# Kernel optimization log

Measured on AMD Instinct MI355X. Metric: run time of the kernel, lower is better.

The kernel has to match this reference:

```python
import jax, jax.numpy as jnp
import numpy as np

D_MODEL = 1024
NUM_HEADS = 16
D_K = D_MODEL // NUM_HEADS


def setup_inputs() -> dict:
    key = jax.random.key(0)
    k1, k2, k3 = jax.random.split(key, 3)
    x = jax.random.normal(k1, (2, 2048, D_MODEL), dtype=jnp.float32)
    # torch Linear(d, 3d): weight shape [3d, d], y = x @ W.T
    W_QKV = jax.random.normal(k2, (3 * D_MODEL, D_MODEL), dtype=jnp.float32) * (1.0 / np.sqrt(D_MODEL))
    W_O = jax.random.normal(k3, (D_MODEL, D_MODEL), dtype=jnp.float32) * (1.0 / np.sqrt(D_MODEL))
    return {"x": x, "W_QKV": W_QKV, "W_O": W_O}


def reference(x, W_QKV, W_O):
    B, T, C = x.shape
    qkv = jnp.einsum('btc,fc->btf', x, W_QKV)  # [B,T,3C]
    q, k, v = jnp.split(qkv, 3, axis=-1)
    def heads(t):
        return t.reshape(B, T, NUM_HEADS, D_K).transpose(0, 2, 1, 3)  # [B,H,T,Dk]
    Q, K, V = heads(q), heads(k), heads(v)
    scores = jnp.einsum('bhqd,bhkd->bhqk', Q, K) / jnp.sqrt(jnp.float32(D_K))
    causal = jnp.tril(jnp.ones((T, T), dtype=bool))
    scores = jnp.where(causal, scores, -jnp.inf)
    attn = jax.nn.softmax(scores, axis=-1)
    out = jnp.einsum('bhqk,bhkd->bhqd', attn, V)
    out = out.transpose(0, 2, 1, 3).reshape(B, T, C)
    return jnp.einsum('btc,oc->bto', out, W_O)
```

## Files before the change

kernel.cpp:

```cpp
#include <hip/hip_runtime.h>
#include <hip/hip_bf16.h>
#include <stdint.h>
#include <stddef.h>


typedef __attribute__((ext_vector_type(8)))  __bf16   bf16x8;
typedef __attribute__((ext_vector_type(4)))  float    f32x4;
typedef __attribute__((ext_vector_type(16))) float    f32x16;
typedef __attribute__((ext_vector_type(4)))  uint32_t u32x4;

#define AS1(p) ((__attribute__((address_space(1))) void*)(p))
#define AS3(p) ((__attribute__((address_space(3))) void*)(p))

static constexpr int Tq    = 2048;
static constexpr int Cd    = 1024;
static constexpr int Mrows = 2 * Tq;

#define QSCALE 0.18033688011112042f

__global__ __launch_bounds__(256) void cvt_bf16_kernel(const float* __restrict__ in,
                                                       __bf16* __restrict__ out, int n8)
{
    int idx    = blockIdx.x * blockDim.x + threadIdx.x;
    int stride = gridDim.x * blockDim.x;
    for (int i = idx; i < n8; i += stride) {
        f32x4 a = ((const f32x4*)in)[i * 2 + 0];
        f32x4 b = ((const f32x4*)in)[i * 2 + 1];
        bf16x8 o;
#pragma unroll
        for (int j = 0; j < 4; ++j) { o[j] = (__bf16)a[j]; o[4 + j] = (__bf16)b[j]; }
        ((bf16x8*)out)[i] = o;
    }
}

__global__ __launch_bounds__(256) void transpose_v_kernel(const __bf16* __restrict__ qkv,
                                                          __bf16* __restrict__ vT)
{
    __shared__ __bf16 tile[64][65];
    const int t   = threadIdx.x;
    const int r0  = blockIdx.x * 64;
    const int hd0 = blockIdx.y * 64;

    {
        const int rr = t >> 2, c16 = (t & 3) * 16;
        const __bf16* src = qkv + (size_t)(r0 + rr) * 3072 + 2048 + hd0 + c16;
        bf16x8 a = *(const bf16x8*)(src);
        bf16x8 b = *(const bf16x8*)(src + 8);
#pragma unroll
        for (int j = 0; j < 8; ++j) { tile[rr][c16 + j] = a[j]; tile[rr][c16 + 8 + j] = b[j]; }
    }
    __syncthreads();
    {
        const int hd_loc = t >> 2, rg = (t & 3) * 16;
        bf16x8 a, b;
#pragma unroll
        for (int j = 0; j < 8; ++j) { a[j] = tile[rg + j][hd_loc]; b[j] = tile[rg + 8 + j][hd_loc]; }
        __bf16* dst = vT + (size_t)(hd0 + hd_loc) * Mrows + r0 + rg;
        *(bf16x8*)(dst)     = a;
        *(bf16x8*)(dst + 8) = b;
    }
}

template <bool OUT_BF16>
__global__ __launch_bounds__(256) void gemm_bt_kernel(const __bf16* __restrict__ A,
                                                      const __bf16* __restrict__ Bm,
                                                      float* __restrict__ Cf,
                                                      __bf16* __restrict__ Cb,
                                                      int N, int K, int qcols, float qscale)
{
    __shared__ __align__(16) __bf16 As[128 * 64];
    __shared__ __align__(16) __bf16 Bs[128 * 64];

    const int tid = threadIdx.x;
    const int l   = tid & 63;
    const int w   = tid >> 6;
    const int wr  = w >> 1, wc = w & 1;
    const int lo  = l & 15, hi = l >> 4;
    const int m0  = blockIdx.x * 128;
    const int n0  = blockIdx.y * 128;

    f32x4 acc[4][4] = {};

    for (int kk = 0; kk < K; kk += 64) {
#pragma unroll
        for (int i = 0; i < 4; ++i) {
            int s   = i * 256 + tid;
            int row = s >> 3;
            int gg  = (s & 7) ^ (row & 7);
            const __bf16* srcA = A  + (size_t)(m0 + row) * K + kk + gg * 8;
            const __bf16* srcB = Bm + (size_t)(n0 + row) * K + kk + gg * 8;
            __builtin_amdgcn_global_load_lds(AS1(srcA), AS3((char*)As + s * 16), 16, 0, 0);
            __builtin_amdgcn_global_load_lds(AS1(srcB), AS3((char*)Bs + s * 16), 16, 0, 0);
        }
        __syncthreads();

#pragma unroll
        for (int ks = 0; ks < 2; ++ks) {
            bf16x8 af[4], bfr[4];
#pragma unroll
            for (int m = 0; m < 4; ++m) {
                int row = wr * 64 + m * 16 + lo;
                int gl  = (ks * 4 + hi) ^ (row & 7);
                af[m] = *(const bf16x8*)((const char*)As + row * 128 + gl * 16);
            }
#pragma unroll
            for (int n = 0; n < 4; ++n) {
                int row = wc * 64 + n * 16 + lo;
                int gl  = (ks * 4 + hi) ^ (row & 7);
                bfr[n] = *(const bf16x8*)((const char*)Bs + row * 128 + gl * 16);
            }
#pragma unroll
            for (int m = 0; m < 4; ++m)
#pragma unroll
                for (int n = 0; n < 4; ++n)
                    acc[m][n] = __builtin_amdgcn_mfma_f32_16x16x32_bf16(af[m], bfr[n], acc[m][n], 0, 0, 0);
        }
        __syncthreads();
    }

#pragma unroll
    for (int m = 0; m < 4; ++m)
#pragma unroll
        for (int n = 0; n < 4; ++n)
#pragma unroll
            for (int r = 0; r < 4; ++r) {
                int row = m0 + wr * 64 + m * 16 + hi * 4 + r;
                int col = n0 + wc * 64 + n * 16 + lo;
                float v = acc[m][n][r];
                if (col < qcols) v *= qscale;
                if (OUT_BF16) Cb[(size_t)row * N + col] = (__bf16)v;
                else          Cf[(size_t)row * N + col] = v;
            }
}

__global__ __launch_bounds__(128) void attn_kernel(const __bf16* __restrict__ qkv,
                                                   const __bf16* __restrict__ vT,
                                                   __bf16* __restrict__ att)
{
    __shared__ __align__(16) __bf16 Ks[2][64 * 64];
    __shared__ __align__(16) __bf16 Vs[2][64 * 64];

    const int tid = threadIdx.x;
    const int l   = tid & 63;
    const int w   = tid >> 6;
    const int lo5 = l & 31, hi5 = l >> 5;

    const int bid = blockIdx.x;
    const int j   = bid & 15;
    const int h   = (bid >> 4) & 15;
    const int b   = bid >> 8;

    const __bf16* Kbase = qkv + (size_t)b * Tq * 3072 + 1024 + h * 64;
    const __bf16* Vbase = vT  + (size_t)h * 64 * Mrows + b * Tq;

    const int qts[2] = {31 - j, j};

    for (int p = 0; p < 2; ++p) {
        const int qt  = qts[p];
        const int qb0 = qt * 64;
        const int nt  = qt + 1;

        bf16x8 qf[4];
        {
            const __bf16* Qp = qkv + (size_t)(b * Tq + qb0 + w * 32 + lo5) * 3072 + h * 64 + hi5 * 8;
#pragma unroll
            for (int ds = 0; ds < 4; ++ds) qf[ds] = *(const bf16x8*)(Qp + ds * 16);
        }

        f32x16 o0 = {}, o1 = {};
        float m = -1e30f, lsum = 0.f;

#pragma unroll
        for (int i = 0; i < 4; ++i) {
            int s = i * 128 + tid;
            int row = s >> 3, g = (s & 7) ^ (row & 7);
            __builtin_amdgcn_global_load_lds(AS1(Kbase + (size_t)row * 3072 + g * 8),
                                             AS3((char*)Ks[0] + s * 16), 16, 0, 0);
            __builtin_amdgcn_global_load_lds(AS1(Vbase + (size_t)row * Mrows + g * 8),
                                             AS3((char*)Vs[0] + s * 16), 16, 0, 0);
        }
        __syncthreads();

        int cur = 0;
        for (int t = 0; t < nt; ++t) {
            const int k0 = t * 64;

            if (t + 1 < nt) {
                const int kn = k0 + 64;
#pragma unroll
                for (int i = 0; i < 4; ++i) {
                    int s = i * 128 + tid;
                    int row = s >> 3, g = (s & 7) ^ (row & 7);
                    __builtin_amdgcn_global_load_lds(AS1(Kbase + (size_t)(kn + row) * 3072 + g * 8),
                                                     AS3((char*)Ks[cur ^ 1] + s * 16), 16, 0, 0);
                    __builtin_amdgcn_global_load_lds(AS1(Vbase + (size_t)row * Mrows + kn + g * 8),
                                                     AS3((char*)Vs[cur ^ 1] + s * 16), 16, 0, 0);
                }
            }

            f32x16 sf0 = {}, sf1 = {};
#pragma unroll
            for (int ds = 0; ds < 4; ++ds) {
                {
                    int row = lo5;
                    int gl  = (ds * 2 + hi5) ^ (row & 7);
                    bf16x8 kf = *(const bf16x8*)((const char*)Ks[cur] + row * 128 + gl * 16);
                    sf0 = __builtin_amdgcn_mfma_f32_32x32x16_bf16(kf, qf[ds], sf0, 0, 0, 0);
                }
                {
                    int row = 32 + lo5;
                    int gl  = (ds * 2 + hi5) ^ (row & 7);
                    bf16x8 kf = *(const bf16x8*)((const char*)Ks[cur] + row * 128 + gl * 16);
                    sf1 = __builtin_amdgcn_mfma_f32_32x32x16_bf16(kf, qf[ds], sf1, 0, 0, 0);
                }
            }

            if (t == qt) {
                const int ql = w * 32 + lo5;
#pragma unroll
                for (int r = 0; r < 16; ++r) {
                    int kc = (r & 3) + 8 * (r >> 2) + 4 * hi5;
                    if (kc      > ql) sf0[r] = -1e30f;
                    if (kc + 32 > ql) sf1[r] = -1e30f;
                }
            }

            float pmh = fmaxf(sf0[0], sf0[1]);
#pragma unroll
            for (int r = 2; r < 16; ++r) pmh = fmaxf(pmh, sf0[r]);
#pragma unroll
            for (int r = 0; r < 16; ++r) pmh = fmaxf(pmh, sf1[r]);
            float pm = fmaxf(pmh, __shfl_xor(pmh, 32));

            if (__any(pm > m + 8.0f)) {
                float mnew = fmaxf(m, pm);
                float fac  = exp2f(m - mnew);
                m = mnew;
                lsum *= fac;
#pragma unroll
                for (int r = 0; r < 16; ++r) {
                    int qreg = (r & 3) + 8 * (r >> 2) + 4 * hi5;
                    float fr = __shfl(fac, qreg);
                    o0[r] *= fr;
                    o1[r] *= fr;
                }
            }

            float psum = 0.f;
#pragma unroll
            for (int kb = 0; kb < 2; ++kb) {
                uint32_t W[8];
#pragma unroll
                for (int wd = 0; wd < 8; ++wd) {
                    float sa = (kb == 0) ? sf0[2 * wd]     : sf1[2 * wd];
                    float sb = (kb == 0) ? sf0[2 * wd + 1] : sf1[2 * wd + 1];
                    float pa = exp2f(sa - m);
                    float pb = exp2f(sb - m);
                    __bf16 ba = (__bf16)pa, bb = (__bf16)pb;
                    psum += (float)ba + (float)bb;
                    W[wd] = (uint32_t)__builtin_bit_cast(uint16_t, ba)
                          | ((uint32_t)__builtin_bit_cast(uint16_t, bb) << 16);
                }
                uint32_t Za = __shfl_xor(hi5 ? W[0] : W[2], 32);
                uint32_t Zb = __shfl_xor(hi5 ? W[1] : W[3], 32);
                uint32_t Zc = __shfl_xor(hi5 ? W[4] : W[6], 32);
                uint32_t Zd = __shfl_xor(hi5 ? W[5] : W[7], 32);

                {
                    u32x4 fw = { hi5 ? Za : W[0], hi5 ? Zb : W[1],
                                 hi5 ? W[2] : Za, hi5 ? W[3] : Zb };
                    bf16x8 pa = __builtin_bit_cast(bf16x8, fw);
                    const int kstep = kb * 2;
                    {
                        int row = lo5;
                        int gl  = (kstep * 2 + hi5) ^ (row & 7);
                        bf16x8 vb = *(const bf16x8*)((const char*)Vs[cur] + row * 128 + gl * 16);
                        o0 = __builtin_amdgcn_mfma_f32_32x32x16_bf16(pa, vb, o0, 0, 0, 0);
                    }
                    {
                        int row = 32 + lo5;
                        int gl  = (kstep * 2 + hi5) ^ (row & 7);
                        bf16x8 vb = *(const bf16x8*)((const char*)Vs[cur] + row * 128 + gl * 16);
                        o1 = __builtin_amdgcn_mfma_f32_32x32x16_bf16(pa, vb, o1, 0, 0, 0);
                    }
                }
                {
                    u32x4 fw = { hi5 ? Zc : W[4], hi5 ? Zd : W[5],
                                 hi5 ? W[6] : Zc, hi5 ? W[7] : Zd };
                    bf16x8 pa = __builtin_bit_cast(bf16x8, fw);
                    const int kstep = kb * 2 + 1;
                    {
                        int row = lo5;
                        int gl  = (kstep * 2 + hi5) ^ (row & 7);
                        bf16x8 vb = *(const bf16x8*)((const char*)Vs[cur] + row * 128 + gl * 16);
                        o0 = __builtin_amdgcn_mfma_f32_32x32x16_bf16(pa, vb, o0, 0, 0, 0);
                    }
                    {
                        int row = 32 + lo5;
                        int gl  = (kstep * 2 + hi5) ^ (row & 7);
                        bf16x8 vb = *(const bf16x8*)((const char*)Vs[cur] + row * 128 + gl * 16);
                        o1 = __builtin_amdgcn_mfma_f32_32x32x16_bf16(pa, vb, o1, 0, 0, 0);
                    }
                }
            }
            psum += __shfl_xor(psum, 32);
            lsum += psum;

            __syncthreads();
            cur ^= 1;
        }

        float linv = 1.0f / lsum;
#pragma unroll
        for (int r = 0; r < 16; ++r) {
            int   qreg = (r & 3) + 8 * (r >> 2) + 4 * hi5;
            float lr   = __shfl(linv, qreg);
            int   rowg = b * Tq + qb0 + w * 32 + qreg;
            att[(size_t)rowg * Cd + h * 64 + lo5]      = (__bf16)(o0[r] * lr);
            att[(size_t)rowg * Cd + h * 64 + 32 + lo5] = (__bf16)(o1[r] * lr);
        }
    }
}

extern "C" void kernel_launch(void* const* d_in, const int* in_sizes, int n_in,
                              void* d_out, int out_size, void* d_ws, size_t ws_size,
                              hipStream_t stream)
{
    (void)in_sizes; (void)n_in; (void)out_size; (void)ws_size;

    const float* x    = (const float*)d_in[0];
    const float* Wqkv = (const float*)d_in[1];
    const float* Wo   = (const float*)d_in[2];
    float*       out  = (float*)d_out;

    char* ws = (char*)d_ws;
    __bf16* xb    = (__bf16*)(ws);
    __bf16* wqkvb = (__bf16*)(ws + (size_t)8  * 1024 * 1024);
    __bf16* wob   = (__bf16*)(ws + (size_t)14 * 1024 * 1024);
    __bf16* qkvb  = (__bf16*)(ws + (size_t)16 * 1024 * 1024);
    __bf16* attb  = (__bf16*)(ws + (size_t)40 * 1024 * 1024);
    __bf16* vTb   = xb;

    cvt_bf16_kernel<<<2048, 256, 0, stream>>>(x,    xb,    Mrows * Cd / 8);
    cvt_bf16_kernel<<<1536, 256, 0, stream>>>(Wqkv, wqkvb, 3 * Cd * Cd / 8);
    cvt_bf16_kernel<<<512,  256, 0, stream>>>(Wo,   wob,   Cd * Cd / 8);

    dim3 g1(Mrows / 128, 3 * Cd / 128);
    gemm_bt_kernel<true><<<g1, 256, 0, stream>>>(xb, wqkvb, nullptr, qkvb, 3 * Cd, Cd,
                                                 1024, QSCALE);

    dim3 gt(Mrows / 64, Cd / 64);
    transpose_v_kernel<<<gt, 256, 0, stream>>>(qkvb, vTb);

    attn_kernel<<<512, 128, 0, stream>>>(qkvb, vTb, attb);

    dim3 g2(Mrows / 128, Cd / 128);
    gemm_bt_kernel<false><<<g2, 256, 0, stream>>>(attb, wob, out, nullptr, Cd, Cd,
                                                  0, 1.0f);
}
```

Baseline: 214.7 us.

## Split attention into one query tile per block, MFMA row sums, setprio

Each attention block now handles a single query tile instead of a paired long/short tile, doubling the grid to 1024 blocks. The query tiles are ordered so the longest causal tiles are scheduled first. The softmax denominator is accumulated with an extra MFMA against a ones vector, replacing scalar adds and shuffles, and the final reciprocal uses rcp. The change also adds s_setprio around the MFMA regions, uses native exp2, and tree-reduces the row max. The trade-off is losing the paired work balancing, relying instead on ordering plus more blocks, and paying extra MFMA work for the row sums.

```diff
diff --git a/kernel.cpp b/kernel.cpp
--- a/kernel.cpp
+++ b/kernel.cpp
@@ -146,179 +146,190 @@
     const int lo5 = l & 31, hi5 = l >> 5;
 
     const int bid = blockIdx.x;
-    const int j   = bid & 15;
-    const int h   = (bid >> 4) & 15;
-    const int b   = bid >> 8;
+    const int g   = (bid >> 5) & 7;
+    const int c   = bid >> 8;
+    const int qt  = (c & 1) ? (16 - ((c >> 1) << 4) + g)
+                            : (31 - ((c >> 1) << 4) - g);
+    const int bh  = bid & 31;
+    const int h   = bh & 15;
+    const int b   = bh >> 4;
 
     const __bf16* Kbase = qkv + (size_t)b * Tq * 3072 + 1024 + h * 64;
     const __bf16* Vbase = vT  + (size_t)h * 64 * Mrows + b * Tq;
 
-    const int qts[2] = {31 - j, j};
-
-    for (int p = 0; p < 2; ++p) {
-        const int qt  = qts[p];
-        const int qb0 = qt * 64;
-        const int nt  = qt + 1;
-
-        bf16x8 qf[4];
-        {
-            const __bf16* Qp = qkv + (size_t)(b * Tq + qb0 + w * 32 + lo5) * 3072 + h * 64 + hi5 * 8;
-#pragma unroll
-            for (int ds = 0; ds < 4; ++ds) qf[ds] = *(const bf16x8*)(Qp + ds * 16);
-        }
-
-        f32x16 o0 = {}, o1 = {};
-        float m = -1e30f, lsum = 0.f;
-
-#pragma unroll
-        for (int i = 0; i < 4; ++i) {
-            int s = i * 128 + tid;
-            int row = s >> 3, g = (s & 7) ^ (row & 7);
-            __builtin_amdgcn_global_load_lds(AS1(Kbase + (size_t)row * 3072 + g * 8),
-                                             AS3((char*)Ks[0] + s * 16), 16, 0, 0);
-            __builtin_amdgcn_global_load_lds(AS1(Vbase + (size_t)row * Mrows + g * 8),
-                                             AS3((char*)Vs[0] + s * 16), 16, 0, 0);
-        }
-        __syncthreads();
-
-        int cur = 0;
-        for (int t = 0; t < nt; ++t) {
-            const int k0 = t * 64;
-
-            if (t + 1 < nt) {
-                const int kn = k0 + 64;
-#pragma unroll
-                for (int i = 0; i < 4; ++i) {
-                    int s = i * 128 + tid;
-                    int row = s >> 3, g = (s & 7) ^ (row & 7);
-                    __builtin_amdgcn_global_load_lds(AS1(Kbase + (size_t)(kn + row) * 3072 + g * 8),
-                                                     AS3((char*)Ks[cur ^ 1] + s * 16), 16, 0, 0);
-                    __builtin_amdgcn_global_load_lds(AS1(Vbase + (size_t)row * Mrows + kn + g * 8),
-                                                     AS3((char*)Vs[cur ^ 1] + s * 16), 16, 0, 0);
-                }
-            }
-
-            f32x16 sf0 = {}, sf1 = {};
-#pragma unroll
-            for (int ds = 0; ds < 4; ++ds) {
+    const int qb0 = qt * 64;
+    const int nt  = qt + 1;
+
+    bf16x8 onesf;
+#pragma unroll
+    for (int jj = 0; jj < 8; ++jj) onesf[jj] = (__bf16)1.0f;
+
+    bf16x8 qf[4];
+    {
+        const __bf16* Qp = qkv + (size_t)(b * Tq + qb0 + w * 32 + lo5) * 3072 + h * 64 + hi5 * 8;
+#pragma unroll
+        for (int ds = 0; ds < 4; ++ds) qf[ds] = *(const bf16x8*)(Qp + ds * 16);
+    }
+
+    f32x16 o0 = {}, o1 = {}, ls = {};
+    float m = -1e30f;
+
+#pragma unroll
+    for (int i = 0; i < 4; ++i) {
+        int s = i * 128 + tid;
+        int row = s >> 3, gg = (s & 7) ^ (row & 7);
+        __builtin_amdgcn_global_load_lds(AS1(Kbase + (size_t)row * 3072 + gg * 8),
+                                         AS3((char*)Ks[0] + s * 16), 16, 0, 0);
+        __builtin_amdgcn_global_load_lds(AS1(Vbase + (size_t)row * Mrows + gg * 8),
+                                         AS3((char*)Vs[0] + s * 16), 16, 0, 0);
+    }
+    __syncthreads();
+
+    int cur = 0;
+    for (int t = 0; t < nt; ++t) {
+        if (t + 1 < nt) {
+            const int kn = (t + 1) * 64;
+#pragma unroll
+            for (int i = 0; i < 4; ++i) {
+                int s = i * 128 + tid;
+                int row = s >> 3, gg = (s & 7) ^ (row & 7);
+                __builtin_amdgcn_global_load_lds(AS1(Kbase + (size_t)(kn + row) * 3072 + gg * 8),
+                                                 AS3((char*)Ks[cur ^ 1] + s * 16), 16, 0, 0);
+                __builtin_amdgcn_global_load_lds(AS1(Vbase + (size_t)row * Mrows + kn + gg * 8),
+                                                 AS3((char*)Vs[cur ^ 1] + s * 16), 16, 0, 0);
+            }
+        }
+
+        f32x16 sf0 = {}, sf1 = {};
+        __builtin_amdgcn_s_setprio(1);
+#pragma unroll
+        for (int ds = 0; ds < 4; ++ds) {
+            {
+                int row = lo5;
+                int gl  = (ds * 2 + hi5) ^ (row & 7);
+                bf16x8 kf = *(const bf16x8*)((const char*)Ks[cur] + row * 128 + gl * 16);
+                sf0 = __builtin_amdgcn_mfma_f32_32x32x16_bf16(kf, qf[ds], sf0, 0, 0, 0);
+            }
+            {
+                int row = 32 + lo5;
+                int gl  = (ds * 2 + hi5) ^ (row & 7);
+                bf16x8 kf = *(const bf16x8*)((const char*)Ks[cur] + row * 128 + gl * 16);
+                sf1 = __builtin_amdgcn_mfma_f32_32x32x16_bf16(kf, qf[ds], sf1, 0, 0, 0);
+            }
+        }
+        __builtin_amdgcn_s_setprio(0);
+
+        if (t == qt) {
+            const int ql = w * 32 + lo5;
+#pragma unroll
+            for (int r = 0; r < 16; ++r) {
+                int kc = (r & 3) + 8 * (r >> 2) + 4 * hi5;
+                if (kc      > ql) sf0[r] = -1e30f;
+                if (kc + 32 > ql) sf1[r] = -1e30f;
+            }
+        }
+
+        float t0 = fmaxf(sf0[0],  fmaxf(sf0[1],  sf0[2]));
+        float t1 = fmaxf(sf0[3],  fmaxf(sf0[4],  sf0[5]));
+        float t2 = fmaxf(sf0[6],  fmaxf(sf0[7],  sf0[8]));
+        float t3 = fmaxf(sf0[9],  fmaxf(sf0[10], sf0[11]));
+        float t4 = fmaxf(sf0[12], fmaxf(sf0[13], sf0[14]));
+        float t5 = fmaxf(sf1[0],  fmaxf(sf1[1],  sf1[2]));
+        float t6 = fmaxf(sf1[3],  fmaxf(sf1[4],  sf1[5]));
+        float t7 = fmaxf(sf1[6],  fmaxf(sf1[7],  sf1[8]));
+        float t8 = fmaxf(sf1[9],  fmaxf(sf1[10], sf1[11]));
+        float t9 = fmaxf(sf1[12], fmaxf(sf1[13], sf1[14]));
+        float u0 = fmaxf(t0, fmaxf(t1, t2));
+        float u1 = fmaxf(t3, fmaxf(t4, sf0[15]));
+        float u2 = fmaxf(t5, fmaxf(t6, t7));
+        float u3 = fmaxf(t8, fmaxf(t9, sf1[15]));
+        float pmh = fmaxf(fmaxf(u0, u1), fmaxf(u2, u3));
+        float pm  = fmaxf(pmh, __shfl_xor(pmh, 32));
+
+        if (__any(pm > m + 8.0f)) {
+            float mnew = fmaxf(m, pm);
+            float fac  = __builtin_amdgcn_exp2f(m - mnew);
+            m = mnew;
+#pragma unroll
+            for (int r = 0; r < 16; ++r) {
+                int qreg = (r & 3) + 8 * (r >> 2) + 4 * hi5;
+                float fr = __shfl(fac, qreg);
+                o0[r] *= fr;
+                o1[r] *= fr;
+                ls[r] *= fr;
+            }
+        }
+
+        __builtin_amdgcn_s_setprio(1);
+#pragma unroll
+        for (int kb = 0; kb < 2; ++kb) {
+            uint32_t W[8];
+#pragma unroll
+            for (int wd = 0; wd < 8; ++wd) {
+                float sa = (kb == 0) ? sf0[2 * wd]     : sf1[2 * wd];
+                float sb = (kb == 0) ? sf0[2 * wd + 1] : sf1[2 * wd + 1];
+                __bf16 ba = (__bf16)__builtin_amdgcn_exp2f(sa - m);
+                __bf16 bb = (__bf16)__builtin_amdgcn_exp2f(sb - m);
+                W[wd] = (uint32_t)__builtin_bit_cast(uint16_t, ba)
+                      | ((uint32_t)__builtin_bit_cast(uint16_t, bb) << 16);
+            }
+            uint32_t Za = __shfl_xor(hi5 ? W[0] : W[2], 32);
+            uint32_t Zb = __shfl_xor(hi5 ? W[1] : W[3], 32);
+            uint32_t Zc = __shfl_xor(hi5 ? W[4] : W[6], 32);
+            uint32_t Zd = __shfl_xor(hi5 ? W[5] : W[7], 32);
+
+            {
+                u32x4 fw = { hi5 ? Za : W[0], hi5 ? Zb : W[1],
+                             hi5 ? W[2] : Za, hi5 ? W[3] : Zb };
+                bf16x8 pa = __builtin_bit_cast(bf16x8, fw);
+                const int kstep = kb * 2;
                 {
                     int row = lo5;
-                    int gl  = (ds * 2 + hi5) ^ (row & 7);
-                    bf16x8 kf = *(const bf16x8*)((const char*)Ks[cur] + row * 128 + gl * 16);
-                    sf0 = __builtin_amdgcn_mfma_f32_32x32x16_bf16(kf, qf[ds], sf0, 0, 0, 0);
+                    int gl  = (kstep * 2 + hi5) ^ (row & 7);
+                    bf16x8 vb = *(const bf16x8*)((const char*)Vs[cur] + row * 128 + gl * 16);
+                    o0 = __builtin_amdgcn_mfma_f32_32x32x16_bf16(pa, vb, o0, 0, 0, 0);
                 }
                 {
                     int row = 32 + lo5;
-                    int gl  = (ds * 2 + hi5) ^ (row & 7);
-                    bf16x8 kf = *(const bf16x8*)((const char*)Ks[cur] + row * 128 + gl * 16);
-                    sf1 = __builtin_amdgcn_mfma_f32_32x32x16_bf16(kf, qf[ds], sf1, 0, 0, 0);
+                    int gl  = (kstep * 2 + hi5) ^ (row & 7);
+                    bf16x8 vb = *(const bf16x8*)((const char*)Vs[cur] + row * 128 + gl * 16);
+                    o1 = __builtin_amdgcn_mfma_f32_32x32x16_bf16(pa, vb, o1, 0, 0, 0);
                 }
-            }
-
-            if (t == qt) {
-                const int ql = w * 32 + lo5;
-#pragma unroll
-                for (int r = 0; r < 16; ++r) {
-                    int kc = (r & 3) + 8 * (r >> 2) + 4 * hi5;
-                    if (kc      > ql) sf0[r] = -1e30f;
-                    if (kc + 32 > ql) sf1[r] = -1e30f;
-                }
-            }
-
-            float pmh = fmaxf(sf0[0], sf0[1]);
-#pragma unroll
-            for (int r = 2; r < 16; ++r) pmh = fmaxf(pmh, sf0[r]);
-#pragma unroll
-            for (int r = 0; r < 16; ++r) pmh = fmaxf(pmh, sf1[r]);
-            float pm = fmaxf(pmh, __shfl_xor(pmh, 32));
-
-            if (__any(pm > m + 8.0f)) {
-                float mnew = fmaxf(m, pm);
-                float fac  = exp2f(m - mnew);
-                m = mnew;
-                lsum *= fac;
-#pragma unroll
-                for (int r = 0; r < 16; ++r) {
-                    int qreg = (r & 3) + 8 * (r >> 2) + 4 * hi5;
-                    float fr = __shfl(fac, qreg);
-                    o0[r] *= fr;
-                    o1[r] *= fr;
-                }
-            }
-
-            float psum = 0.f;
-#pragma unroll
-            for (int kb = 0; kb < 2; ++kb) {
-                uint32_t W[8];
-#pragma unroll
-                for (int wd = 0; wd < 8; ++wd) {
-                    float sa = (kb == 0) ? sf0[2 * wd]     : sf1[2 * wd];
-                    float sb = (kb == 0) ? sf0[2 * wd + 1] : sf1[2 * wd + 1];
-                    float pa = exp2f(sa - m);
-                    float pb = exp2f(sb - m);
-                    __bf16 ba = (__bf16)pa, bb = (__bf16)pb;
-                    psum += (float)ba + (float)bb;
-                    W[wd] = (uint32_t)__builtin_bit_cast(uint16_t, ba)
-                          | ((uint32_t)__builtin_bit_cast(uint16_t, bb) << 16);
-                }
-                uint32_t Za = __shfl_xor(hi5 ? W[0] : W[2], 32);
-                uint32_t Zb = __shfl_xor(hi5 ? W[1] : W[3], 32);
-                uint32_t Zc = __shfl_xor(hi5 ? W[4] : W[6], 32);
-                uint32_t Zd = __shfl_xor(hi5 ? W[5] : W[7], 32);
-
+                ls = __builtin_amdgcn_mfma_f32_32x32x16_bf16(pa, onesf, ls, 0, 0, 0);
+            }
+            {
+                u32x4 fw = { hi5 ? Zc : W[4], hi5 ? Zd : W[5],
+                             hi5 ? W[6] : Zc, hi5 ? W[7] : Zd };
+                bf16x8 pa = __builtin_bit_cast(bf16x8, fw);
+                const int kstep = kb * 2 + 1;
                 {
-                    u32x4 fw = { hi5 ? Za : W[0], hi5 ? Zb : W[1],
-                                 hi5 ? W[2] : Za, hi5 ? W[3] : Zb };
-                    bf16x8 pa = __builtin_bit_cast(bf16x8, fw);
-                    const int kstep = kb * 2;
-                    {
-                        int row = lo5;
-                        int gl  = (kstep * 2 + hi5) ^ (row & 7);
-                        bf16x8 vb = *(const bf16x8*)((const char*)Vs[cur] + row * 128 + gl * 16);
-                        o0 = __builtin_amdgcn_mfma_f32_32x32x16_bf16(pa, vb, o0, 0, 0, 0);
-                    }
-                    {
-                        int row = 32 + lo5;
-                        int gl  = (kstep * 2 + hi5) ^ (row & 7);
-                        bf16x8 vb = *(const bf16x8*)((const char*)Vs[cur] + row * 128 + gl * 16);
-                        o1 = __builtin_amdgcn_mfma_f32_32x32x16_bf16(pa, vb, o1, 0, 0, 0);
-                    }
+                    int row = lo5;
+                    int gl  = (kstep * 2 + hi5) ^ (row & 7);
+                    bf16x8 vb = *(const bf16x8*)((const char*)Vs[cur] + row * 128 + gl * 16);
+                    o0 = __builtin_amdgcn_mfma_f32_32x32x16_bf16(pa, vb, o0, 0, 0, 0);
                 }
                 {
-                    u32x4 fw = { hi5 ? Zc : W[4], hi5 ? Zd : W[5],
-                                 hi5 ? W[6] : Zc, hi5 ? W[7] : Zd };
-                    bf16x8 pa = __builtin_bit_cast(bf16x8, fw);
-                    const int kstep = kb * 2 + 1;
-                    {
-                        int row = lo5;
-                        int gl  = (kstep * 2 + hi5) ^ (row & 7);
-                        bf16x8 vb = *(const bf16x8*)((const char*)Vs[cur] + row * 128 + gl * 16);
-                        o0 = __builtin_amdgcn_mfma_f32_32x32x16_bf16(pa, vb, o0, 0, 0, 0);
-                    }
-                    {
-                        int row = 32 + lo5;
-                        int gl  = (kstep * 2 + hi5) ^ (row & 7);
-                        bf16x8 vb = *(const bf16x8*)((const char*)Vs[cur] + row * 128 + gl * 16);
-                        o1 = __builtin_amdgcn_mfma_f32_32x32x16_bf16(pa, vb, o1, 0, 0, 0);
-                    }
+                    int row = 32 + lo5;
+                    int gl  = (kstep * 2 + hi5) ^ (row & 7);
+                    bf16x8 vb = *(const bf16x8*)((const char*)Vs[cur] + row * 128 + gl * 16);
+                    o1 = __builtin_amdgcn_mfma_f32_32x32x16_bf16(pa, vb, o1, 0, 0, 0);
                 }
-            }
-            psum += __shfl_xor(psum, 32);
-            lsum += psum;
-
-            __syncthreads();
-            cur ^= 1;
-        }
-
-        float linv = 1.0f / lsum;
-#pragma unroll
-        for (int r = 0; r < 16; ++r) {
-            int   qreg = (r & 3) + 8 * (r >> 2) + 4 * hi5;
-            float lr   = __shfl(linv, qreg);
-            int   rowg = b * Tq + qb0 + w * 32 + qreg;
-            att[(size_t)rowg * Cd + h * 64 + lo5]      = (__bf16)(o0[r] * lr);
-            att[(size_t)rowg * Cd + h * 64 + 32 + lo5] = (__bf16)(o1[r] * lr);
-        }
+                ls = __builtin_amdgcn_mfma_f32_32x32x16_bf16(pa, onesf, ls, 0, 0, 0);
+            }
+        }
+        __builtin_amdgcn_s_setprio(0);
+
+        __syncthreads();
+        cur ^= 1;
+    }
+
+#pragma unroll
+    for (int r = 0; r < 16; ++r) {
+        float lr   = __builtin_amdgcn_rcpf(ls[r]);
+        int   qreg = (r & 3) + 8 * (r >> 2) + 4 * hi5;
+        int   rowg = b * Tq + qb0 + w * 32 + qreg;
+        att[(size_t)rowg * Cd + h * 64 + lo5]      = (__bf16)(o0[r] * lr);
+        att[(size_t)rowg * Cd + h * 64 + 32 + lo5] = (__bf16)(o1[r] * lr);
     }
 }
 
@@ -352,7 +363,7 @@
     dim3 gt(Mrows / 64, Cd / 64);
     transpose_v_kernel<<<gt, 256, 0, stream>>>(qkvb, vTb);
 
-    attn_kernel<<<512, 128, 0, stream>>>(qkvb, vTb, attb);
+    attn_kernel<<<1024, 128, 0, stream>>>(qkvb, vTb, attb);
 
     dim3 g2(Mrows / 128, Cd / 128);
     gemm_bt_kernel<false><<<g2, 256, 0, stream>>>(attb, wob, out, nullptr, Cd, Cd,
```

New measurement: 206.2 us. 1.04x faster.
